# Kernel optimization log

Measured on AMD Instinct MI355X. Metric: run time of the kernel, lower is better.

Reference implementation:

```python
import jax, jax.numpy as jnp
from jax import lax
import numpy as np

S, B, T, N, FJ, H, MF, M = 8, 64, 64, 16, 32, 128, 16, 8
NN = S + M  # total machine-graph nodes
EPS = 1e-5
SLOPE = 0.2


def layernorm(x, g, b):
    mu = x.mean(-1, keepdims=True)
    var = ((x - mu) ** 2).mean(-1, keepdims=True)
    return (x - mu) / jnp.sqrt(var + EPS) * g + b


def gat(adj, x, W, a):
    # dense GAT layer: x [..., N, Fin], adj [..., N, N]
    h = x @ W  # [..., N, O]
    O = W.shape[1]
    f1 = h @ a[:O]  # [..., N]
    f2 = h @ a[O:]
    e = jax.nn.leaky_relu(f1[..., :, None] + f2[..., None, :], SLOPE)
    e = jnp.where(adj > 0, e, jnp.float32(-1e9))
    return jax.nn.softmax(e, axis=-1) @ h


def job_enc(adj, x, Ws, As):
    t = jnp.tanh(gat(adj, x, Ws[0], As[0]))
    t = jnp.tanh(gat(adj, t, Ws[1], As[1]) + t)
    t = jnp.tanh(gat(adj, t, Ws[2], As[2]) + t)
    t = jnp.tanh(t + gat(adj, t, Ws[3], As[3]))
    return t.mean(-2)  # mean over ops dim


def lstm_last(x, Wih, Whh, b):
    # x: [Bx, T, H]; returns final hidden state [Bx, H]
    xs = jnp.einsum('bti,gi->tbg', x, Wih) + b  # [T, Bx, 4H]
    h0 = jnp.zeros((x.shape[0], Whh.shape[1]), x.dtype)

    def step(carry, xt):
        h, c = carry
        g = xt + h @ Whh.T
        i, f, gg, o = jnp.split(g, 4, axis=-1)
        c = jax.nn.sigmoid(f) * c + jax.nn.sigmoid(i) * jnp.tanh(gg)
        h = jax.nn.sigmoid(o) * jnp.tanh(c)
        return (h, c), None

    (h, _), _ = lax.scan(step, (h0, h0), xs)
    return h


def setup_inputs() -> dict:
    key = jax.random.key(0)
    ks = jax.random.split(key, 32)

    def adj(k, shape):
        a = jax.random.bernoulli(k, 0.4, shape).astype(jnp.int32)
        return jnp.maximum(a, jnp.eye(shape[-1], dtype=jnp.int32))

    mfeat = jax.random.normal(ks[4], (B, NN, MF), jnp.float32)
    # stage nodes (first S) have feature[...,0] > 0; machine nodes < 0
    mfeat = mfeat.at[:, :S, 0].set(jnp.abs(mfeat[:, :S, 0]) + 0.1)
    mfeat = mfeat.at[:, S:, 0].set(-jnp.abs(mfeat[:, S:, 0]) - 0.1)

    sc = 0.08
    inp = {
        'j_stages_f': jax.random.normal(ks[0], (S, B, T, N, FJ), jnp.float32),
        'j_stages_a': adj(ks[1], (S, B, T, N, N)),
        'j_machine_f': jax.random.normal(ks[2], (B, M, N, FJ), jnp.float32),
        'j_machine_a': adj(ks[3], (B, M, N, N)),
        'machine_f': mfeat,
        'machine_a': adj(ks[5], (B, NN, NN)),
        'jg1_W': jax.random.normal(ks[6], (FJ, H), jnp.float32) * sc,
        'jgW': jax.random.normal(ks[7], (3, H, H), jnp.float32) * sc,
        'jga': jax.random.normal(ks[8], (4, 2 * H), jnp.float32) * sc,
        'lstm_Wih': jax.random.normal(ks[9], (4 * H, H), jnp.float32) * sc,
        'lstm_Whh': jax.random.normal(ks[10], (4 * H, H), jnp.float32) * sc,
        'lstm_b': jnp.zeros((4 * H,), jnp.float32),
        'mfe_W': jax.random.normal(ks[11], (MF, H), jnp.float32) * sc,
        'mfe_b': jnp.zeros((H,), jnp.float32),
        'n2_g': jnp.ones((H,), jnp.float32),
        'n2_b': jnp.zeros((H,), jnp.float32),
        'me_W': jax.random.normal(ks[12], (2 * H, H), jnp.float32) * sc,
        'me_b': jnp.zeros((H,), jnp.float32),
        'n3_g': jnp.ones((H,), jnp.float32),
        'n3_b': jnp.zeros((H,), jnp.float32),
        'mgW': jax.random.normal(ks[13], (4, H, H), jnp.float32) * sc,
        'mga': jax.random.normal(ks[14], (4, 2 * H), jnp.float32) * sc,
        'mng': jnp.ones((4, H), jnp.float32),
        'mnb': jnp.zeros((4, H), jnp.float32),
    }
    return inp


def reference(j_stages_f, j_stages_a, j_machine_f, j_machine_a, machine_f,
              machine_a, jg1_W, jgW, jga, lstm_Wih, lstm_Whh, lstm_b,
              mfe_W, mfe_b, n2_g, n2_b, me_W, me_b, n3_g, n3_b,
              mgW, mga, mng, mnb):
    Ws = [jg1_W, jgW[0], jgW[1], jgW[2]]
    As = [jga[0], jga[1], jga[2], jga[3]]

    # per-stage job encoding + LSTM over job sequence
    stage_emb = jax.vmap(lambda a, f: job_enc(a, f, Ws, As))(j_stages_a, j_stages_f)  # [S,B,T,H]
    hlast = lstm_last(stage_emb.reshape(S * B, T, H), lstm_Wih, lstm_Whh, lstm_b)
    j_encoded = hlast.reshape(S, B, H).transpose(1, 0, 2)  # [B,S,H]

    # machine-side job graph encoding (shared encoder)
    jm = job_enc(j_machine_a, j_machine_f, Ws, As)  # [B,M,H]

    # machine node embedding
    mfh = jnp.tanh(layernorm(machine_f @ mfe_W + mfe_b, n2_g, n2_b))  # [B,NN,H]

    # static routing: first S nodes -> stage contexts, rest -> machine contexts
    ctx = jnp.concatenate([j_encoded, jm], axis=1)  # [B,NN,H]
    nodes = jnp.concatenate([mfh, ctx], axis=-1)  # [B,NN,2H]
    nodes = jnp.tanh(layernorm(nodes @ me_W + me_b, n3_g, n3_b))

    h = nodes
    prev = None
    for k in range(4):
        h2 = layernorm(gat(machine_a, h, mgW[k], mga[k]), mng[k], mnb[k])
        if k != 0:
            h2 = h2 + prev
        h = jnp.tanh(h2)
        prev = h
    return h.mean(axis=1)  # [B, H]
```

## Files before the change

### kernel.cpp

```cpp
#include <hip/hip_runtime.h>
#include <hip/hip_bf16.h>
#include <math.h>

#define S_ 8
#define B_ 64
#define T_ 64
#define N_ 16
#define FJ_ 32
#define H_ 128
#define MF_ 16
#define M_ 8
#define SB_ 512
#define G1_ 32768
#define G2_ 512

#define CPAD 132
#define PPAD 17

typedef short bf16x8 __attribute__((ext_vector_type(8)));
typedef short bf16x4 __attribute__((ext_vector_type(4)));
typedef float f32x4 __attribute__((ext_vector_type(4)));
typedef unsigned short u16;

__device__ __forceinline__ u16 f2bf(float f) {
  union { float f; unsigned u; } v; v.f = f;
  unsigned r = v.u + 0x7FFFu + ((v.u >> 16) & 1u);
  return (u16)(r >> 16);
}
__device__ __forceinline__ unsigned pk2(float lo, float hi) {
  __hip_bfloat162 h2 = __float22bfloat162_rn(make_float2(lo, hi));
  union { __hip_bfloat162 h; unsigned u; } x; x.h = h2; return x.u;
}
__device__ __forceinline__ bf16x4 mkfrag(unsigned a, unsigned b) {
  union { bf16x4 v; unsigned u[2]; } x; x.u[0] = a; x.u[1] = b; return x.v;
}
__device__ __forceinline__ f32x4 mfma16(bf16x4 a, bf16x4 b, f32x4 c) {
#if __has_builtin(__builtin_amdgcn_mfma_f32_16x16x16bf16_1k)
  return __builtin_amdgcn_mfma_f32_16x16x16bf16_1k(a, b, c, 0, 0, 0);
#else
  asm("v_mfma_f32_16x16x16_bf16 %0, %1, %2, %0" : "+v"(c) : "v"(a), "v"(b));
  return c;
#endif
}
__device__ __forceinline__ float frcp(float x) {
#if __has_builtin(__builtin_amdgcn_rcpf)
  return __builtin_amdgcn_rcpf(x);
#else
  return 1.f / x;
#endif
}
__device__ __forceinline__ float frsq(float x) {
#if __has_builtin(__builtin_amdgcn_rsqf)
  return __builtin_amdgcn_rsqf(x);
#else
  return rsqrtf(x);
#endif
}
__device__ __forceinline__ float ftanh(float x) {
  float e = __expf(2.f * x);
  return fmaf(-2.f, frcp(e + 1.f), 1.f);
}
__device__ __forceinline__ float sigmoidf_(float x) {
  return frcp(1.f + __expf(-x));
}

__device__ __forceinline__ void fma8(float (&acc)[8], float xv, float4 wa, float4 wb) {
  acc[0] = fmaf(xv, wa.x, acc[0]); acc[1] = fmaf(xv, wa.y, acc[1]);
  acc[2] = fmaf(xv, wa.z, acc[2]); acc[3] = fmaf(xv, wa.w, acc[3]);
  acc[4] = fmaf(xv, wb.x, acc[4]); acc[5] = fmaf(xv, wb.y, acc[5]);
  acc[6] = fmaf(xv, wb.z, acc[6]); acc[7] = fmaf(xv, wb.w, acc[7]);
}
__device__ __forceinline__ float grp16_sum(float v) {
#pragma unroll
  for (int m = 1; m < 16; m <<= 1) v += __shfl_xor(v, m);
  return v;
}
__device__ __forceinline__ float grp16_max(float v) {
#pragma unroll
  for (int m = 1; m < 16; m <<= 1) v = fmaxf(v, __shfl_xor(v, m));
  return v;
}
__device__ __forceinline__ void ln_row(float (&v)[8], const float* gw, const float* bw, int j0) {
  float s1 = 0.f, s2 = 0.f;
#pragma unroll
  for (int c = 0; c < 8; ++c) { s1 += v[c]; s2 += v[c] * v[c]; }
  s1 = grp16_sum(s1); s2 = grp16_sum(s2);
  float mu = s1 * (1.f / 128.f);
  float var = s2 * (1.f / 128.f) - mu * mu;
  float rstd = frsq(var + 1e-5f);
#pragma unroll
  for (int c = 0; c < 8; ++c) v[c] = (v[c] - mu) * rstd * gw[j0 + c] + bw[j0 + c];
}

__global__ __launch_bounds__(256) void pack_w_kernel(
    const float* __restrict__ W0, const float* __restrict__ W123,
    const float* __restrict__ jga,
    const float* __restrict__ Wih, const float* __restrict__ Whh,
    u16* __restrict__ wpk0, u16* __restrict__ wpkL,
    u16* __restrict__ wpkIH, u16* __restrict__ wpkHH)
{
  int idx = blockIdx.x * 256 + threadIdx.x;
  if (idx < 4608) {
    int e = idx & 3, l = (idx >> 2) & 63, t = idx >> 8;
    int n = t >> 1, kk = t & 1;
    int q = l >> 4, cc = l & 15;
    int k = 16 * kk + 4 * q + e;
    float v = 0.f;
    if (n < 8) v = W0[k * 128 + 16 * n + cc];
    else if (cc < 2) {
      const float* a = jga + cc * 128;
      float s = 0.f;
      for (int j = 0; j < 128; ++j) s += W0[k * 128 + j] * a[j];
      v = s;
    }
    wpk0[idx] = f2bf(v);
  } else if (idx < 59904) {
    int id = idx - 4608;
    int e = id & 3, l = (id >> 2) & 63;
    int t2 = id >> 8;
    int t = t2 % 72, layer = t2 / 72;
    int n = t >> 3, kk = t & 7;
    int q = l >> 4, cc = l & 15;
    int k = 16 * kk + 4 * q + e;
    const float* W = W123 + (size_t)layer * 16384;
    float v = 0.f;
    if (n < 8) v = W[k * 128 + 16 * n + cc];
    else if (cc < 2) {
      const float* a = jga + (layer + 1) * 256 + cc * 128;
      float s = 0.f;
      for (int j = 0; j < 128; ++j) s += W[k * 128 + j] * a[j];
      v = s;
    }
    wpkL[id] = f2bf(v);
  } else if (idx < 125440) {
    int id = idx - 59904;
    int e = id & 7, l = (id >> 3) & 63, kk = (id >> 9) & 3, n = id >> 11;
    int gate = 16 * n + (l & 15), k = 32 * kk + 8 * (l >> 4) + e;
    wpkIH[id] = f2bf(Wih[gate * 128 + k]);
  } else if (idx < 190976) {
    int id = idx - 125440;
    int e = id & 7, l = (id >> 3) & 63, kk = (id >> 9) & 3, n = id >> 11;
    int gate = 16 * n + (l & 15), k = 32 * kk + 8 * (l >> 4) + e;
    wpkHH[id] = f2bf(Whh[gate * 128 + k]);
  }
}

__global__ __launch_bounds__(1024) __attribute__((amdgpu_waves_per_eu(4, 8)))
void gat_mfma_kernel(
    const float* __restrict__ xinA, const int* __restrict__ adjA,
    float* __restrict__ outmA, u16* __restrict__ outbfA,
    const float* __restrict__ xinB, const int* __restrict__ adjB,
    float* __restrict__ outmB, u16* __restrict__ outbfB,
    const u16* __restrict__ wpk0, const u16* __restrict__ wpkL)
{
  __shared__ __align__(16) u16 wbuf[18432];
  __shared__ __align__(16) float fbuf[16][32];

  const int tid = threadIdx.x;
  const int wv = tid >> 6;
  const int l = tid & 63;
  const int c = l & 15, q = l >> 4;
  float* fb = fbuf[wv];

  const float* xin; const int* adjin; float* outm; u16* outbf; int g;
  if (blockIdx.x < G1_ / 16) {
    xin = xinA; adjin = adjA; outm = outmA; outbf = outbfA;
    g = blockIdx.x * 16 + wv;
  } else {
    xin = xinB; adjin = adjB; outm = outmB; outbf = outbfB;
    g = (blockIdx.x - G1_ / 16) * 16 + wv;
  }

  auto stage = [&](const u16* src, int nbytes) {
    const float4* s4 = (const float4*)src;
    float4* d4 = (float4*)wbuf;
    int n16 = nbytes >> 4;
    for (int i = tid; i < n16; i += 1024) d4[i] = s4[i];
  };

  int4 A1 = *(const int4*)(adjin + (size_t)g * 256 + c * 16 + 4 * q);

  f32x4 res[8];
  bf16x4 hfrag[8];

  auto softmax_pv = [&](f32x4 Cf, bool resid) {
    if (c < 2) *(f32x4*)(fb + c * 16 + 4 * q) = Cf;
    float f1v = fb[c];
    float4 f2v = *(const float4*)(fb + 16 + 4 * q);
    float ev[4] = {f1v + f2v.x, f1v + f2v.y, f1v + f2v.z, f1v + f2v.w};
#pragma unroll
    for (int e = 0; e < 4; ++e) ev[e] = (ev[e] >= 0.f) ? ev[e] : 0.2f * ev[e];
    ev[0] = (A1.x > 0) ? ev[0] : -1e9f;
    ev[1] = (A1.y > 0) ? ev[1] : -1e9f;
    ev[2] = (A1.z > 0) ? ev[2] : -1e9f;
    ev[3] = (A1.w > 0) ? ev[3] : -1e9f;
    float mx = fmaxf(fmaxf(ev[0], ev[1]), fmaxf(ev[2], ev[3]));
    mx = fmaxf(mx, __shfl_xor(mx, 16));
    mx = fmaxf(mx, __shfl_xor(mx, 32));
    float sm = 0.f;
#pragma unroll
    for (int e = 0; e < 4; ++e) { ev[e] = __expf(ev[e] - mx); sm += ev[e]; }
    sm += __shfl_xor(sm, 16);
    sm += __shfl_xor(sm, 32);
    float zinv = frcp(sm);
    bf16x4 pfrag = mkfrag(pk2(ev[0] * zinv, ev[1] * zinv), pk2(ev[2] * zinv, ev[3] * zinv));
#pragma unroll
    for (int m = 0; m < 8; ++m) {
      f32x4 o = resid ? res[m] : (f32x4){0.f, 0.f, 0.f, 0.f};
      o = mfma16(hfrag[m], pfrag, o);
      f32x4 t;
      t[0] = ftanh(o[0]); t[1] = ftanh(o[1]); t[2] = ftanh(o[2]); t[3] = ftanh(o[3]);
      res[m] = t;
    }
  };

  stage(wpk0, 9216);
  __syncthreads();
  {
    bf16x4 xf[2];
    const float* xg = xin + (size_t)g * 512 + c * 32 + 4 * q;
    float4 x1 = *(const float4*)xg;
    float4 x2 = *(const float4*)(xg + 16);
    xf[0] = mkfrag(pk2(x1.x, x1.y), pk2(x1.z, x1.w));
    xf[1] = mkfrag(pk2(x2.x, x2.y), pk2(x2.z, x2.w));
#pragma unroll
    for (int n = 0; n < 8; ++n) {
      f32x4 Ch = (f32x4){0.f, 0.f, 0.f, 0.f};
#pragma unroll
      for (int kk = 0; kk < 2; ++kk) {
        bf16x4 wf = *(const bf16x4*)(wbuf + ((n * 2 + kk) * 64 + l) * 4);
        Ch = mfma16(xf[kk], wf, Ch);
      }
      hfrag[n] = mkfrag(pk2(Ch[0], Ch[1]), pk2(Ch[2], Ch[3]));
    }
    f32x4 Cf = (f32x4){0.f, 0.f, 0.f, 0.f};
#pragma unroll
    for (int kk = 0; kk < 2; ++kk) {
      bf16x4 wf = *(const bf16x4*)(wbuf + ((16 + kk) * 64 + l) * 4);
      Cf = mfma16(xf[kk], wf, Cf);
    }
    softmax_pv(Cf, false);
  }
  __syncthreads();

#pragma unroll 1
  for (int layer = 1; layer < 4; ++layer) {
    stage(wpkL + (size_t)(layer - 1) * 18432, 36864);
    __syncthreads();
    bf16x4 xf[8];
#pragma unroll
    for (int kk = 0; kk < 8; ++kk)
      xf[kk] = mkfrag(pk2(res[kk][0], res[kk][1]), pk2(res[kk][2], res[kk][3]));
#pragma unroll
    for (int n = 0; n < 8; ++n) {
      f32x4 Ch = (f32x4){0.f, 0.f, 0.f, 0.f};
#pragma unroll
      for (int kk = 0; kk < 8; ++kk) {
        bf16x4 wf = *(const bf16x4*)(wbuf + ((n * 8 + kk) * 64 + l) * 4);
        Ch = mfma16(xf[kk], wf, Ch);
      }
      hfrag[n] = mkfrag(pk2(Ch[0], Ch[1]), pk2(Ch[2], Ch[3]));
    }
    f32x4 Cf = (f32x4){0.f, 0.f, 0.f, 0.f};
#pragma unroll
    for (int kk = 0; kk < 8; ++kk) {
      bf16x4 wf = *(const bf16x4*)(wbuf + ((64 + kk) * 64 + l) * 4);
      Cf = mfma16(xf[kk], wf, Cf);
    }
    softmax_pv(Cf, true);
    __syncthreads();
  }

  u16* tb = wbuf + (wv & 7) * 2176;
  auto epi = [&]() {
#pragma unroll
    for (int m = 0; m < 8; ++m) {
      uint2 u;
      u.x = pk2(res[m][0], res[m][1]);
      u.y = pk2(res[m][2], res[m][3]);
      *(uint2*)(tb + c * 136 + 16 * m + 4 * q) = u;
    }
    float s0 = 0.f, s1 = 0.f;
#pragma unroll
    for (int node = 0; node < 16; ++node) {
      unsigned u = *(const unsigned*)(tb + node * 136 + 2 * l);
      union { unsigned u; float f; } lo, hi;
      lo.u = u << 16; hi.u = u & 0xffff0000u;
      s0 += lo.f; s1 += hi.f;
    }
    s0 *= 0.0625f; s1 *= 0.0625f;
    if (outm) *(float2*)(outm + (size_t)g * 128 + 2 * l) = make_float2(s0, s1);
    *(unsigned*)(outbf + (size_t)g * 128 + 2 * l) = pk2(s0, s1);
  };
  if (wv < 8) epi();
  __syncthreads();
  if (wv >= 8) epi();
}

__global__ __launch_bounds__(512) __attribute__((amdgpu_waves_per_eu(1, 2)))
void lstm_fused_kernel(
    const u16* __restrict__ emb_bf,
    const u16* __restrict__ wpkIH, const u16* __restrict__ wpkHH,
    const float* __restrict__ bvec,
    float* __restrict__ hlast)
{
  __shared__ unsigned hbuf[2][1024];
  const int tid = threadIdx.x;
  const int w = tid >> 6, l = tid & 63;
  const int c = l & 15, q = l >> 4;
  const int ce = c & 7;
  const int seq0 = blockIdx.x * 8;
  const int swz = (c & 7) << 2;

  bf16x8 aih[4][4], ahh[4][4];
#pragma unroll
  for (int m = 0; m < 4; ++m)
#pragma unroll
    for (int kk = 0; kk < 4; ++kk) {
      int n = 8 * m + w;
      aih[m][kk] = *(const bf16x8*)(wpkIH + ((size_t)((n * 4 + kk) * 64 + l)) * 8);
      ahh[m][kk] = *(const bf16x8*)(wpkHH + ((size_t)((n * 4 + kk) * 64 + l)) * 8);
    }
  float bias[4][4];
#pragma unroll
  for (int m = 0; m < 4; ++m)
#pragma unroll
    for (int r = 0; r < 4; ++r) bias[m][r] = bvec[128 * m + 16 * w + 4 * q + r];

  hbuf[0][tid] = 0u;
  hbuf[0][512 + tid] = 0u;
  __syncthreads();

  const u16* xbase = emb_bf + ((size_t)(seq0 + ce)) * 64 * 128 + q * 8;

  bf16x8 xnxt[4];
  f32x4 accih[4];
  {
    bf16x8 xf[4];
#pragma unroll
    for (int kk = 0; kk < 4; ++kk) xf[kk] = *(const bf16x8*)(xbase + kk * 32);
#pragma unroll
    for (int m = 0; m < 4; ++m) {
      f32x4 a = (f32x4){0.f, 0.f, 0.f, 0.f};
#pragma unroll
      for (int kk = 0; kk < 4; ++kk)
        a = __builtin_amdgcn_mfma_f32_16x16x32_bf16(aih[m][kk], xf[kk], a, 0, 0, 0);
      accih[m] = a;
    }
#pragma unroll
    for (int kk = 0; kk < 4; ++kk) xnxt[kk] = *(const bf16x8*)(xbase + 128 + kk * 32);
  }

  float cst[4] = {0.f, 0.f, 0.f, 0.f};
  float hv[4] = {0.f, 0.f, 0.f, 0.f};
  int pb = 0;
#pragma unroll 1
  for (int t = 0; t < T_; ++t) {
    bf16x8 hf[4];
#pragma unroll
    for (int kk = 0; kk < 4; ++kk) {
      int j0 = (16 * kk + 4 * q) ^ swz;
      hf[kk] = *(const bf16x8*)&hbuf[pb][c * 64 + j0];
    }
    f32x4 acc[4];
#pragma unroll
    for (int m = 0; m < 4; ++m) {
      f32x4 a = accih[m];
#pragma unroll
      for (int kk = 0; kk < 4; ++kk)
        a = __builtin_amdgcn_mfma_f32_16x16x32_bf16(ahh[m][kk], hf[kk], a, 0, 0, 0);
      acc[m] = a;
    }
#pragma unroll
    for (int r = 0; r < 4; ++r) {
      float ig = acc[0][r] + bias[0][r];
      float fg = acc[1][r] + bias[1][r];
      float gg = acc[2][r] + bias[2][r];
      float og = acc[3][r] + bias[3][r];
      cst[r] = sigmoidf_(fg) * cst[r] + sigmoidf_(ig) * ftanh(gg);
      hv[r] = sigmoidf_(og) * ftanh(cst[r]);
    }
    {
      int j0 = (8 * w + 2 * q) ^ swz;
      uint2 u2; u2.x = pk2(hv[0], hv[1]); u2.y = pk2(hv[2], hv[3]);
      *(uint2*)&hbuf[pb ^ 1][c * 64 + j0] = u2;
    }
    if (t < T_ - 1) {
#pragma unroll
      for (int m = 0; m < 4; ++m) {
        f32x4 a = (f32x4){0.f, 0.f, 0.f, 0.f};
#pragma unroll
        for (int kk = 0; kk < 4; ++kk)
          a = __builtin_amdgcn_mfma_f32_16x16x32_bf16(aih[m][kk], xnxt[kk], a, 0, 0, 0);
        accih[m] = a;
      }
      if (t < T_ - 2) {
        const u16* xr = xbase + (size_t)(t + 2) * 128;
#pragma unroll
        for (int kk = 0; kk < 4; ++kk) xnxt[kk] = *(const bf16x8*)(xr + kk * 32);
      }
    }
    __syncthreads();
    pb ^= 1;
  }
  if (c < 8) {
#pragma unroll
    for (int r = 0; r < 4; ++r)
      hlast[((size_t)(seq0 + ce)) * 128 + 16 * w + 4 * q + r] = hv[r];
  }
}

__global__ __launch_bounds__(256) __attribute__((amdgpu_waves_per_eu(2, 4)))
void machine_kernel(
    const float* __restrict__ machine_f, const int* __restrict__ machine_a,
    const float* __restrict__ hlast, const float* __restrict__ jm,
    const float* __restrict__ mfe_W, const float* __restrict__ mfe_b,
    const float* __restrict__ n2_g, const float* __restrict__ n2_b,
    const float* __restrict__ me_W, const float* __restrict__ me_b,
    const float* __restrict__ n3_g, const float* __restrict__ n3_b,
    const float* __restrict__ mgW, const float* __restrict__ mga,
    const float* __restrict__ mng, const float* __restrict__ mnb,
    float* __restrict__ outp)
{
  __shared__ float mf[256];
  __shared__ int adjs[256];
  __shared__ __align__(16) float ctx[16 * CPAD];
  __shared__ __align__(16) float mfh[16 * CPAD];
  __shared__ __align__(16) float cur[16 * CPAD];
  __shared__ __align__(16) float tmp[16 * CPAD];
  __shared__ __align__(16) float prevb[16 * CPAD];
  __shared__ float pm[16 * PPAD];
  __shared__ float f1s[16], f2s[16];

  const int b = blockIdx.x;
  const int tid = threadIdx.x;
  const int i = tid >> 4;
  const int jb = tid & 15;
  const int j0 = jb << 3;

  mf[tid] = machine_f[(size_t)b * 256 + tid];
  adjs[tid] = machine_a[(size_t)b * 256 + tid];
  {
    const float* src = (i < 8) ? (hlast + ((size_t)i * B_ + b) * H_)
                               : (jm + ((size_t)b * M_ + (i - 8)) * H_);
    *(float4*)(ctx + i * CPAD + j0) = ((const float4*)src)[jb * 2];
    *(float4*)(ctx + i * CPAD + j0 + 4) = ((const float4*)src)[jb * 2 + 1];
  }
  __syncthreads();

  {
    float acc[8];
#pragma unroll
    for (int c = 0; c < 8; ++c) acc[c] = 0.f;
#pragma unroll
    for (int k = 0; k < MF_; ++k) {
      float xv = mf[i * 16 + k];
      float4 wa = *(const float4*)(mfe_W + (size_t)k * H_ + j0);
      float4 wb = *(const float4*)(mfe_W + (size_t)k * H_ + j0 + 4);
      fma8(acc, xv, wa, wb);
    }
#pragma unroll
    for (int c = 0; c < 8; ++c) acc[c] += mfe_b[j0 + c];
    ln_row(acc, n2_g, n2_b, j0);
#pragma unroll
    for (int c = 0; c < 8; ++c) mfh[i * CPAD + j0 + c] = ftanh(acc[c]);
  }
  __syncthreads();

  {
    float acc[8];
#pragma unroll
    for (int c = 0; c < 8; ++c) acc[c] = 0.f;
#pragma unroll 4
    for (int k = 0; k < H_; ++k) {
      float xv = mfh[i * CPAD + k];
      float4 wa = *(const float4*)(me_W + (size_t)k * H_ + j0);
      float4 wb = *(const float4*)(me_W + (size_t)k * H_ + j0 + 4);
      fma8(acc, xv, wa, wb);
    }
#pragma unroll 4
    for (int k = 0; k < H_; ++k) {
      float xv = ctx[i * CPAD + k];
      float4 wa = *(const float4*)(me_W + (size_t)(128 + k) * H_ + j0);
      float4 wb = *(const float4*)(me_W + (size_t)(128 + k) * H_ + j0 + 4);
      fma8(acc, xv, wa, wb);
    }
#pragma unroll
    for (int c = 0; c < 8; ++c) acc[c] += me_b[j0 + c];
    ln_row(acc, n3_g, n3_b, j0);
#pragma unroll
    for (int c = 0; c < 8; ++c) cur[i * CPAD + j0 + c] = ftanh(acc[c]);
  }
  __syncthreads();

  for (int ll = 0; ll < 4; ++ll) {
    const float* W = mgW + (size_t)ll * H_ * H_;
    const float* a0 = mga + ll * 256;
    const float* a1 = a0 + 128;

    float acc[8];
#pragma unroll
    for (int c = 0; c < 8; ++c) acc[c] = 0.f;
#pragma unroll 4
    for (int k = 0; k < H_; ++k) {
      float xv = cur[i * CPAD + k];
      float4 wa = *(const float4*)(W + (size_t)k * H_ + j0);
      float4 wb = *(const float4*)(W + (size_t)k * H_ + j0 + 4);
      fma8(acc, xv, wa, wb);
    }
    *(float4*)(tmp + i * CPAD + j0) = make_float4(acc[0], acc[1], acc[2], acc[3]);
    *(float4*)(tmp + i * CPAD + j0 + 4) = make_float4(acc[4], acc[5], acc[6], acc[7]);

    float p1 = 0.f, p2 = 0.f;
#pragma unroll
    for (int c = 0; c < 8; ++c) {
      p1 = fmaf(acc[c], a0[j0 + c], p1);
      p2 = fmaf(acc[c], a1[j0 + c], p2);
    }
    p1 = grp16_sum(p1); p2 = grp16_sum(p2);
    if (jb == 0) { f1s[i] = p1; f2s[i] = p2; }
    __syncthreads();

    {
      int jc = jb;
      float e = f1s[i] + f2s[jc];
      e = (e >= 0.f) ? e : 0.2f * e;
      if (adjs[i * 16 + jc] <= 0) e = -1e9f;
      float mxv = grp16_max(e);
      float ex = __expf(e - mxv);
      float smv = grp16_sum(ex);
      pm[i * PPAD + jc] = ex * frcp(smv);
    }
    __syncthreads();

    float o[8];
#pragma unroll
    for (int c = 0; c < 8; ++c) o[c] = 0.f;
#pragma unroll
    for (int k = 0; k < 16; ++k) {
      float pv = pm[i * PPAD + k];
      float4 ha = *(const float4*)(tmp + k * CPAD + j0);
      float4 hb = *(const float4*)(tmp + k * CPAD + j0 + 4);
      fma8(o, pv, ha, hb);
    }
    ln_row(o, mng + ll * H_, mnb + ll * H_, j0);
#pragma unroll
    for (int c = 0; c < 8; ++c) {
      float v = o[c] + ((ll > 0) ? prevb[i * CPAD + j0 + c] : 0.f);
      v = ftanh(v);
      cur[i * CPAD + j0 + c] = v;
      prevb[i * CPAD + j0 + c] = v;
    }
    __syncthreads();
  }

  if (tid < 128) {
    float s = 0.f;
#pragma unroll
    for (int r = 0; r < 16; ++r) s += cur[r * CPAD + tid];
    outp[(size_t)b * H_ + tid] = s * (1.f / 16.f);
  }
}

extern "C" void kernel_launch(void* const* d_in, const int* in_sizes, int n_in,
                              void* d_out, int out_size, void* d_ws, size_t ws_size,
                              hipStream_t stream) {
  const float* j_stages_f  = (const float*)d_in[0];
  const int*   j_stages_a  = (const int*)d_in[1];
  const float* j_machine_f = (const float*)d_in[2];
  const int*   j_machine_a = (const int*)d_in[3];
  const float* machine_f   = (const float*)d_in[4];
  const int*   machine_a   = (const int*)d_in[5];
  const float* jg1_W       = (const float*)d_in[6];
  const float* jgW         = (const float*)d_in[7];
  const float* jga         = (const float*)d_in[8];
  const float* lstm_Wih    = (const float*)d_in[9];
  const float* lstm_Whh    = (const float*)d_in[10];
  const float* lstm_b      = (const float*)d_in[11];
  const float* mfe_W       = (const float*)d_in[12];
  const float* mfe_b       = (const float*)d_in[13];
  const float* n2_g        = (const float*)d_in[14];
  const float* n2_b        = (const float*)d_in[15];
  const float* me_W        = (const float*)d_in[16];
  const float* me_b        = (const float*)d_in[17];
  const float* n3_g        = (const float*)d_in[18];
  const float* n3_b        = (const float*)d_in[19];
  const float* mgW         = (const float*)d_in[20];
  const float* mga         = (const float*)d_in[21];
  const float* mng         = (const float*)d_in[22];
  const float* mnb         = (const float*)d_in[23];
  float* out = (float*)d_out;

  char* ws = (char*)d_ws;
  u16*   emb_bf  = (u16*)ws;
  u16*   jmbf    = (u16*)(ws + 8388608);
  float* jm      = (float*)(ws + 8519680);
  float* hlast   = (float*)(ws + 8781824);
  u16*   wpk0    = (u16*)(ws + 9043968);
  u16*   wpkL    = (u16*)(ws + 9053184);
  u16*   wpkIH   = (u16*)(ws + 9163776);
  u16*   wpkHH   = (u16*)(ws + 9294848);

  pack_w_kernel<<<746, 256, 0, stream>>>(jg1_W, jgW, jga, lstm_Wih, lstm_Whh,
                                         wpk0, wpkL, wpkIH, wpkHH);
  gat_mfma_kernel<<<G1_ / 16 + G2_ / 16, 1024, 0, stream>>>(
      j_stages_f, j_stages_a, (float*)nullptr, emb_bf,
      j_machine_f, j_machine_a, jm, jmbf, wpk0, wpkL);
  lstm_fused_kernel<<<SB_ / 8, 512, 0, stream>>>(emb_bf, wpkIH, wpkHH, lstm_b, hlast);
  machine_kernel<<<B_, 256, 0, stream>>>(machine_f, machine_a, hlast, jm,
                                         mfe_W, mfe_b, n2_g, n2_b, me_W, me_b,
                                         n3_g, n3_b, mgW, mga, mng, mnb, out);
}
```

Measured before the change: 366.7 us.

## Split each GAT graph across two waves with smaller blocks and LDS exchange

New measurement: 376.4 us. +2.6%, slower.

```diff
diff --git a/kernel.cpp b/kernel.cpp
--- a/kernel.cpp
+++ b/kernel.cpp
@@ -145,7 +145,7 @@
   }
 }
 
-__global__ __launch_bounds__(1024) __attribute__((amdgpu_waves_per_eu(4, 8)))
+__global__ __launch_bounds__(512) __attribute__((amdgpu_waves_per_eu(2, 4)))
 void gat_mfma_kernel(
     const float* __restrict__ xinA, const int* __restrict__ adjA,
     float* __restrict__ outmA, u16* __restrict__ outbfA,
@@ -154,37 +154,40 @@
     const u16* __restrict__ wpk0, const u16* __restrict__ wpkL)
 {
   __shared__ __align__(16) u16 wbuf[18432];
-  __shared__ __align__(16) float fbuf[16][32];
+  __shared__ __align__(16) u16 tbuf[4][16 * 136];
+  __shared__ __align__(16) float fbuf[4][32];
 
   const int tid = threadIdx.x;
   const int wv = tid >> 6;
+  const int gi = wv >> 1;
+  const int half = wv & 1;
   const int l = tid & 63;
   const int c = l & 15, q = l >> 4;
-  float* fb = fbuf[wv];
+  float* fb = fbuf[gi];
+  u16* tb = tbuf[gi];
 
   const float* xin; const int* adjin; float* outm; u16* outbf; int g;
-  if (blockIdx.x < G1_ / 16) {
+  if (blockIdx.x < G1_ / 4) {
     xin = xinA; adjin = adjA; outm = outmA; outbf = outbfA;
-    g = blockIdx.x * 16 + wv;
+    g = blockIdx.x * 4 + gi;
   } else {
     xin = xinB; adjin = adjB; outm = outmB; outbf = outbfB;
-    g = (blockIdx.x - G1_ / 16) * 16 + wv;
+    g = (blockIdx.x - G1_ / 4) * 4 + gi;
   }
 
   auto stage = [&](const u16* src, int nbytes) {
     const float4* s4 = (const float4*)src;
     float4* d4 = (float4*)wbuf;
     int n16 = nbytes >> 4;
-    for (int i = tid; i < n16; i += 1024) d4[i] = s4[i];
+    for (int i = tid; i < n16; i += 512) d4[i] = s4[i];
   };
 
   int4 A1 = *(const int4*)(adjin + (size_t)g * 256 + c * 16 + 4 * q);
 
-  f32x4 res[8];
-  bf16x4 hfrag[8];
-
-  auto softmax_pv = [&](f32x4 Cf, bool resid) {
-    if (c < 2) *(f32x4*)(fb + c * 16 + 4 * q) = Cf;
+  f32x4 res[4];
+  bf16x4 hfrag[4];
+
+  auto softmax_pv_store = [&](bool resid) {
     float f1v = fb[c];
     float4 f2v = *(const float4*)(fb + 16 + 4 * q);
     float ev[4] = {f1v + f2v.x, f1v + f2v.y, f1v + f2v.z, f1v + f2v.w};
@@ -205,17 +208,20 @@
     float zinv = frcp(sm);
     bf16x4 pfrag = mkfrag(pk2(ev[0] * zinv, ev[1] * zinv), pk2(ev[2] * zinv, ev[3] * zinv));
 #pragma unroll
-    for (int m = 0; m < 8; ++m) {
-      f32x4 o = resid ? res[m] : (f32x4){0.f, 0.f, 0.f, 0.f};
-      o = mfma16(hfrag[m], pfrag, o);
+    for (int n = 0; n < 4; ++n) {
+      f32x4 o = resid ? res[n] : (f32x4){0.f, 0.f, 0.f, 0.f};
+      o = mfma16(hfrag[n], pfrag, o);
       f32x4 t;
       t[0] = ftanh(o[0]); t[1] = ftanh(o[1]); t[2] = ftanh(o[2]); t[3] = ftanh(o[3]);
-      res[m] = t;
+      res[n] = t;
+      uint2 u;
+      u.x = pk2(t[0], t[1]);
+      u.y = pk2(t[2], t[3]);
+      *(uint2*)(tb + c * 136 + 16 * (4 * half + n) + 4 * q) = u;
     }
   };
 
   stage(wpk0, 9216);
-  __syncthreads();
   {
     bf16x4 xf[2];
     const float* xg = xin + (size_t)g * 512 + c * 32 + 4 * q;
@@ -223,25 +229,30 @@
     float4 x2 = *(const float4*)(xg + 16);
     xf[0] = mkfrag(pk2(x1.x, x1.y), pk2(x1.z, x1.w));
     xf[1] = mkfrag(pk2(x2.x, x2.y), pk2(x2.z, x2.w));
-#pragma unroll
-    for (int n = 0; n < 8; ++n) {
+    __syncthreads();
+#pragma unroll
+    for (int n = 0; n < 4; ++n) {
+      int nn = 4 * half + n;
       f32x4 Ch = (f32x4){0.f, 0.f, 0.f, 0.f};
 #pragma unroll
       for (int kk = 0; kk < 2; ++kk) {
-        bf16x4 wf = *(const bf16x4*)(wbuf + ((n * 2 + kk) * 64 + l) * 4);
+        bf16x4 wf = *(const bf16x4*)(wbuf + ((nn * 2 + kk) * 64 + l) * 4);
         Ch = mfma16(xf[kk], wf, Ch);
       }
       hfrag[n] = mkfrag(pk2(Ch[0], Ch[1]), pk2(Ch[2], Ch[3]));
     }
-    f32x4 Cf = (f32x4){0.f, 0.f, 0.f, 0.f};
-#pragma unroll
-    for (int kk = 0; kk < 2; ++kk) {
-      bf16x4 wf = *(const bf16x4*)(wbuf + ((16 + kk) * 64 + l) * 4);
-      Cf = mfma16(xf[kk], wf, Cf);
-    }
-    softmax_pv(Cf, false);
-  }
-  __syncthreads();
+    if (half == 0) {
+      f32x4 Cf = (f32x4){0.f, 0.f, 0.f, 0.f};
+#pragma unroll
+      for (int kk = 0; kk < 2; ++kk) {
+        bf16x4 wf = *(const bf16x4*)(wbuf + ((16 + kk) * 64 + l) * 4);
+        Cf = mfma16(xf[kk], wf, Cf);
+      }
+      if (c < 2) *(f32x4*)(fb + c * 16 + 4 * q) = Cf;
+    }
+    __syncthreads();
+    softmax_pv_store(false);
+  }
 
 #pragma unroll 1
   for (int layer = 1; layer < 4; ++layer) {
@@ -250,51 +261,45 @@
     bf16x4 xf[8];
 #pragma unroll
     for (int kk = 0; kk < 8; ++kk)
-      xf[kk] = mkfrag(pk2(res[kk][0], res[kk][1]), pk2(res[kk][2], res[kk][3]));
-#pragma unroll
-    for (int n = 0; n < 8; ++n) {
+      xf[kk] = *(const bf16x4*)(tb + c * 136 + 16 * kk + 4 * q);
+#pragma unroll
+    for (int n = 0; n < 4; ++n) {
+      int nn = 4 * half + n;
       f32x4 Ch = (f32x4){0.f, 0.f, 0.f, 0.f};
 #pragma unroll
       for (int kk = 0; kk < 8; ++kk) {
-        bf16x4 wf = *(const bf16x4*)(wbuf + ((n * 8 + kk) * 64 + l) * 4);
+        bf16x4 wf = *(const bf16x4*)(wbuf + ((nn * 8 + kk) * 64 + l) * 4);
         Ch = mfma16(xf[kk], wf, Ch);
       }
       hfrag[n] = mkfrag(pk2(Ch[0], Ch[1]), pk2(Ch[2], Ch[3]));
     }
-    f32x4 Cf = (f32x4){0.f, 0.f, 0.f, 0.f};
-#pragma unroll
-    for (int kk = 0; kk < 8; ++kk) {
-      bf16x4 wf = *(const bf16x4*)(wbuf + ((64 + kk) * 64 + l) * 4);
-      Cf = mfma16(xf[kk], wf, Cf);
-    }
-    softmax_pv(Cf, true);
-    __syncthreads();
-  }
-
-  u16* tb = wbuf + (wv & 7) * 2176;
-  auto epi = [&]() {
-#pragma unroll
-    for (int m = 0; m < 8; ++m) {
-      uint2 u;
-      u.x = pk2(res[m][0], res[m][1]);
-      u.y = pk2(res[m][2], res[m][3]);
-      *(uint2*)(tb + c * 136 + 16 * m + 4 * q) = u;
-    }
-    float s0 = 0.f, s1 = 0.f;
+    if (half == 0) {
+      f32x4 Cf = (f32x4){0.f, 0.f, 0.f, 0.f};
+#pragma unroll
+      for (int kk = 0; kk < 8; ++kk) {
+        bf16x4 wf = *(const bf16x4*)(wbuf + ((64 + kk) * 64 + l) * 4);
+        Cf = mfma16(xf[kk], wf, Cf);
+      }
+      if (c < 2) *(f32x4*)(fb + c * 16 + 4 * q) = Cf;
+    }
+    __syncthreads();
+    softmax_pv_store(true);
+  }
+
+  __syncthreads();
+  {
+    int feat = 64 * half + l;
+    float s = 0.f;
 #pragma unroll
     for (int node = 0; node < 16; ++node) {
-      unsigned u = *(const unsigned*)(tb + node * 136 + 2 * l);
-      union { unsigned u; float f; } lo, hi;
-      lo.u = u << 16; hi.u = u & 0xffff0000u;
-      s0 += lo.f; s1 += hi.f;
-    }
-    s0 *= 0.0625f; s1 *= 0.0625f;
-    if (outm) *(float2*)(outm + (size_t)g * 128 + 2 * l) = make_float2(s0, s1);
-    *(unsigned*)(outbf + (size_t)g * 128 + 2 * l) = pk2(s0, s1);
-  };
-  if (wv < 8) epi();
-  __syncthreads();
-  if (wv >= 8) epi();
+      union { unsigned u; float f; } x;
+      x.u = (unsigned)tb[node * 136 + feat] << 16;
+      s += x.f;
+    }
+    s *= 0.0625f;
+    if (outm) outm[(size_t)g * 128 + feat] = s;
+    outbf[(size_t)g * 128 + feat] = f2bf(s);
+  }
 }
 
 __global__ __launch_bounds__(512) __attribute__((amdgpu_waves_per_eu(1, 2)))
@@ -603,7 +608,7 @@
 
   pack_w_kernel<<<746, 256, 0, stream>>>(jg1_W, jgW, jga, lstm_Wih, lstm_Whh,
                                          wpk0, wpkL, wpkIH, wpkHH);
-  gat_mfma_kernel<<<G1_ / 16 + G2_ / 16, 1024, 0, stream>>>(
+  gat_mfma_kernel<<<G1_ / 4 + G2_ / 4, 512, 0, stream>>>(
       j_stages_f, j_stages_a, (float*)nullptr, emb_bf,
       j_machine_f, j_machine_a, jm, jmbf, wpk0, wpkL);
   lstm_fused_kernel<<<SB_ / 8, 512, 0, stream>>>(emb_bf, wpkIH, wpkHH, lstm_b, hlast);
```
